# Performance work log

Hardware: AMD Instinct MI355X
Metric: run time of the kernel (lower is better)

## Reference

```python
import jax, jax.numpy as jnp
import numpy as np

N_ATOMS = 20000
NN = 64
N_TYPES = 4
N_DESC = 8
K_MAX = 8
R_C = 8.0


def chebyshev_basis(r, r_c, k_max):
    # modified Chebyshev basis with smooth cutoff (NEP)
    fc = jnp.where(r < r_c, 0.5 * jnp.cos(jnp.pi * r / r_c) + 0.5, jnp.zeros_like(r))
    x = 2.0 * (r / r_c - 1.0) ** 2 - 1.0
    fn = [jnp.ones_like(x)]
    if k_max > 1:
        fn.append(x)
        for _ in range(2, k_max):
            fn.append(2.0 * x * fn[-1] - fn[-2])
    fn = jnp.stack(fn, axis=-1)  # [..., k_max]
    return (fn + 1.0) * (0.5 * fc)[..., None]


def setup_inputs() -> dict:
    key = jax.random.key(0)
    k1, k2, k3, k4, k5, k6 = jax.random.split(key, 6)
    types = jax.random.randint(k1, (N_ATOMS,), 0, N_TYPES, dtype=jnp.int32)
    positions = jax.random.normal(k2, (N_ATOMS, 3), dtype=jnp.float32) * 3.0
    neighbors = jax.random.randint(k3, (N_ATOMS, NN), 0, N_ATOMS, dtype=jnp.int32)
    drop = jax.random.uniform(k4, (N_ATOMS, NN)) < 0.1
    radial_neighbors = jnp.where(drop, jnp.int32(-1), neighbors)
    radial_offsets = jax.random.normal(k5, (N_ATOMS, NN, 3), dtype=jnp.float32)
    c_table = jax.random.normal(k6, (N_TYPES, N_TYPES, N_DESC, K_MAX), dtype=jnp.float32)
    return {
        "types": types,
        "positions": positions,
        "radial_neighbors": radial_neighbors,
        "radial_offsets": radial_offsets,
        "c_table": c_table,
    }


def reference(types, positions, radial_neighbors, radial_offsets, c_table):
    mask = radial_neighbors != -1                       # [N, NN]
    safe = jnp.where(mask, radial_neighbors, 0)         # [N, NN]
    # gather neighbor positions, apply periodic offsets
    r_vec = positions[safe] + radial_offsets - positions[:, None, :]  # [N, NN, 3]
    distances = jnp.linalg.norm(r_vec, axis=-1)         # [N, NN]
    f = chebyshev_basis(distances, R_C, K_MAX)          # [N, NN, K]
    coeff = c_table[types[:, None], types[safe]]        # [N, NN, D, K]
    edge_desc = jnp.einsum('ajdk,ajk->ajd', coeff, f)   # [N, NN, D]
    edge_desc = edge_desc * mask[..., None].astype(edge_desc.dtype)
    return edge_desc.sum(axis=1)                        # [N, D]
```

## Files before the change

### kernel.cpp

```cpp
#include <hip/hip_runtime.h>
#include <hip/hip_bf16.h>

#define N_ATOMS_MAX 20000
#define NN 64
#define N_TYPES 4
#define N_DESC 8
#define K_MAX 8
#define R_C 8.0f

__global__ __launch_bounds__(256) void radial_desc_kernel(
    const int* __restrict__ types,
    const float* __restrict__ positions,
    const int* __restrict__ radial_neighbors,
    const float* __restrict__ radial_offsets,
    const float* __restrict__ c_table,
    float* __restrict__ out,
    int n_atoms)
{
    __shared__ float ld_c[N_DESC * K_MAX * N_TYPES * N_TYPES];

    const int tid = threadIdx.x;
    #pragma unroll
    for (int i = tid; i < N_DESC * K_MAX * N_TYPES * N_TYPES; i += 256) {
        const int dk = i >> 4;
        const int tt = i & 15;
        ld_c[i] = c_table[tt * (N_DESC * K_MAX) + dk];
    }
    __syncthreads();

    const int wave = tid >> 6;
    const int lane = tid & 63;
    const int a = blockIdx.x * 4 + wave;
    if (a >= n_atoms) return;

    const int nb = radial_neighbors[a * NN + lane];
    const bool valid = (nb != -1);
    const int safe = valid ? nb : 0;

    const float3 off = *reinterpret_cast<const float3*>(radial_offsets + (size_t)(a * NN + lane) * 3);
    const float3 pn  = *reinterpret_cast<const float3*>(positions + (size_t)safe * 3);
    const float3 pa  = *reinterpret_cast<const float3*>(positions + (size_t)a * 3);

    const int ta = types[a];
    const int tn = types[safe];

    const float dx = pn.x + off.x - pa.x;
    const float dy = pn.y + off.y - pa.y;
    const float dz = pn.z + off.z - pa.z;
    const float r  = sqrtf(dx * dx + dy * dy + dz * dz);

    const float rr = r * (1.0f / R_C);
    const float cosp = __cosf(3.14159265358979323846f * rr);
    const float half_fc = (valid && (r < R_C)) ? (0.25f * cosp + 0.25f) : 0.0f;

    const float x = 2.0f * (rr - 1.0f) * (rr - 1.0f) - 1.0f;

    float fn[K_MAX];
    fn[0] = 1.0f;
    fn[1] = x;
    #pragma unroll
    for (int k = 2; k < K_MAX; ++k)
        fn[k] = 2.0f * x * fn[k - 1] - fn[k - 2];

    float f[K_MAX];
    #pragma unroll
    for (int k = 0; k < K_MAX; ++k)
        f[k] = (fn[k] + 1.0f) * half_fc;

    const int cb = ta * N_TYPES + tn;
    float acc[N_DESC];
    #pragma unroll
    for (int d = 0; d < N_DESC; ++d) {
        float s = 0.0f;
        #pragma unroll
        for (int k = 0; k < K_MAX; ++k)
            s += ld_c[(d * K_MAX + k) * 16 + cb] * f[k];
        acc[d] = s;
    }

    #pragma unroll
    for (int d = 0; d < N_DESC; ++d) {
        float v = acc[d];
        #pragma unroll
        for (int s = 1; s < 64; s <<= 1)
            v += __shfl_xor(v, s, 64);
        acc[d] = v;
    }

    if (lane == 0) {
        float4* o4 = reinterpret_cast<float4*>(out + (size_t)a * N_DESC);
        o4[0] = make_float4(acc[0], acc[1], acc[2], acc[3]);
        o4[1] = make_float4(acc[4], acc[5], acc[6], acc[7]);
    }
}

extern "C" void kernel_launch(void* const* d_in, const int* in_sizes, int n_in,
                              void* d_out, int out_size, void* d_ws, size_t ws_size,
                              hipStream_t stream) {
    const int*   types            = (const int*)d_in[0];
    const float* positions        = (const float*)d_in[1];
    const int*   radial_neighbors = (const int*)d_in[2];
    const float* radial_offsets   = (const float*)d_in[3];
    const float* c_table          = (const float*)d_in[4];
    float* out = (float*)d_out;

    const int n_atoms = in_sizes[0];
    const int blocks = (n_atoms + 3) / 4;
    radial_desc_kernel<<<blocks, 256, 0, stream>>>(
        types, positions, radial_neighbors, radial_offsets, c_table, out, n_atoms);
}
```

Baseline: 94.11 us.

## Pack positions and types into float4 and use transposed partial shuffle reduction

Adds a pre-pass kernel that packs each atom's position and type into one float4 in workspace. The neighbor gather then needs a single 16-byte load instead of separate position and type loads. The per-descriptor butterfly reduction is also restructured: each of the 8 descriptors is reduced across 8 lanes, the results are transposed so each lane holds one descriptor, and three more shuffles finish the sum, which cuts the shuffle count. The cost is an extra kernel launch plus the workspace write and read.

New measurement: 93.13 us. About the same (-1.0%).

```diff
diff --git a/kernel.cpp b/kernel.cpp
--- a/kernel.cpp
+++ b/kernel.cpp
@@ -1,16 +1,26 @@
 #include <hip/hip_runtime.h>
 #include <hip/hip_bf16.h>
 
-#define N_ATOMS_MAX 20000
 #define NN 64
 #define N_TYPES 4
 #define N_DESC 8
 #define K_MAX 8
 #define R_C 8.0f
 
-__global__ __launch_bounds__(256) void radial_desc_kernel(
+__global__ __launch_bounds__(256) void pack_pos_type(
     const int* __restrict__ types,
     const float* __restrict__ positions,
+    float4* __restrict__ packed,
+    int n_atoms)
+{
+    const int a = blockIdx.x * 256 + threadIdx.x;
+    if (a >= n_atoms) return;
+    const float* p = positions + (size_t)a * 3;
+    packed[a] = make_float4(p[0], p[1], p[2], __int_as_float(types[a]));
+}
+
+__global__ __launch_bounds__(256) void radial_desc_kernel(
+    const float4* __restrict__ packed,
     const int* __restrict__ radial_neighbors,
     const float* __restrict__ radial_offsets,
     const float* __restrict__ c_table,
@@ -20,7 +30,6 @@
     __shared__ float ld_c[N_DESC * K_MAX * N_TYPES * N_TYPES];
 
     const int tid = threadIdx.x;
-    #pragma unroll
     for (int i = tid; i < N_DESC * K_MAX * N_TYPES * N_TYPES; i += 256) {
         const int dk = i >> 4;
         const int tt = i & 15;
@@ -34,19 +43,18 @@
     if (a >= n_atoms) return;
 
     const int nb = radial_neighbors[a * NN + lane];
+    const float3 off = *reinterpret_cast<const float3*>(radial_offsets + (size_t)(a * NN + lane) * 3);
+    const float4 pta = packed[a];
     const bool valid = (nb != -1);
     const int safe = valid ? nb : 0;
+    const float4 ptn = packed[safe];
 
-    const float3 off = *reinterpret_cast<const float3*>(radial_offsets + (size_t)(a * NN + lane) * 3);
-    const float3 pn  = *reinterpret_cast<const float3*>(positions + (size_t)safe * 3);
-    const float3 pa  = *reinterpret_cast<const float3*>(positions + (size_t)a * 3);
+    const int ta = __float_as_int(pta.w);
+    const int tn = __float_as_int(ptn.w);
 
-    const int ta = types[a];
-    const int tn = types[safe];
-
-    const float dx = pn.x + off.x - pa.x;
-    const float dy = pn.y + off.y - pa.y;
-    const float dz = pn.z + off.z - pa.z;
+    const float dx = ptn.x + off.x - pta.x;
+    const float dy = ptn.y + off.y - pta.y;
+    const float dz = ptn.z + off.z - pta.z;
     const float r  = sqrtf(dx * dx + dy * dy + dz * dz);
 
     const float rr = r * (1.0f / R_C);
@@ -55,17 +63,16 @@
 
     const float x = 2.0f * (rr - 1.0f) * (rr - 1.0f) - 1.0f;
 
-    float fn[K_MAX];
-    fn[0] = 1.0f;
-    fn[1] = x;
+    float fn0 = 1.0f, fn1 = x;
+    float f[K_MAX];
+    f[0] = (fn0 + 1.0f) * half_fc;
+    f[1] = (fn1 + 1.0f) * half_fc;
     #pragma unroll
-    for (int k = 2; k < K_MAX; ++k)
-        fn[k] = 2.0f * x * fn[k - 1] - fn[k - 2];
-
-    float f[K_MAX];
-    #pragma unroll
-    for (int k = 0; k < K_MAX; ++k)
-        f[k] = (fn[k] + 1.0f) * half_fc;
+    for (int k = 2; k < K_MAX; ++k) {
+        const float fnk = 2.0f * x * fn1 - fn0;
+        f[k] = (fnk + 1.0f) * half_fc;
+        fn0 = fn1; fn1 = fnk;
+    }
 
     const int cb = ta * N_TYPES + tn;
     float acc[N_DESC];
@@ -81,17 +88,21 @@
     #pragma unroll
     for (int d = 0; d < N_DESC; ++d) {
         float v = acc[d];
-        #pragma unroll
-        for (int s = 1; s < 64; s <<= 1)
-            v += __shfl_xor(v, s, 64);
+        v += __shfl_xor(v, 1, 64);
+        v += __shfl_xor(v, 2, 64);
+        v += __shfl_xor(v, 4, 64);
         acc[d] = v;
     }
+    float v = acc[0];
+    #pragma unroll
+    for (int d = 1; d < N_DESC; ++d)
+        v = ((lane & 7) == d) ? acc[d] : v;
+    v += __shfl_xor(v, 8, 64);
+    v += __shfl_xor(v, 16, 64);
+    v += __shfl_xor(v, 32, 64);
 
-    if (lane == 0) {
-        float4* o4 = reinterpret_cast<float4*>(out + (size_t)a * N_DESC);
-        o4[0] = make_float4(acc[0], acc[1], acc[2], acc[3]);
-        o4[1] = make_float4(acc[4], acc[5], acc[6], acc[7]);
-    }
+    if (lane < 8)
+        out[(size_t)a * N_DESC + lane] = v;
 }
 
 extern "C" void kernel_launch(void* const* d_in, const int* in_sizes, int n_in,
@@ -103,9 +114,13 @@
     const float* radial_offsets   = (const float*)d_in[3];
     const float* c_table          = (const float*)d_in[4];
     float* out = (float*)d_out;
+    float4* packed = (float4*)d_ws;
 
     const int n_atoms = in_sizes[0];
-    const int blocks = (n_atoms + 3) / 4;
-    radial_desc_kernel<<<blocks, 256, 0, stream>>>(
-        types, positions, radial_neighbors, radial_offsets, c_table, out, n_atoms);
+
+    pack_pos_type<<<(n_atoms + 255) / 256, 256, 0, stream>>>(
+        types, positions, packed, n_atoms);
+
+    radial_desc_kernel<<<(n_atoms + 3) / 4, 256, 0, stream>>>(
+        packed, radial_neighbors, radial_offsets, c_table, out, n_atoms);
 }
```
